# Kernel tuning notes

Hardware: AMD Instinct MI355X
Metric: run time of the kernel (lower is better)

## Reference

```python
import jax, jax.numpy as jnp
import numpy as np

EMB = 512
HEADS = 8
HEAD_DIM = EMB // HEADS


def setup_inputs() -> dict:
    key = jax.random.key(0)
    ks = jax.random.split(key, 8)
    S, B = 2048, 2
    q = jax.random.normal(ks[0], (S, B, EMB), dtype=jnp.float32)
    k = jax.random.normal(ks[1], (S, B, EMB), dtype=jnp.float32)
    v = jax.random.normal(ks[2], (S, B, EMB), dtype=jnp.float32)
    sc = 1.0 / np.sqrt(HEAD_DIM)
    Wq = jax.random.normal(ks[3], (HEAD_DIM, HEAD_DIM), dtype=jnp.float32) * sc
    Wk = jax.random.normal(ks[4], (HEAD_DIM, HEAD_DIM), dtype=jnp.float32) * sc
    Wv = jax.random.normal(ks[5], (HEAD_DIM, HEAD_DIM), dtype=jnp.float32) * sc
    Wfc = jax.random.normal(ks[6], (EMB, EMB), dtype=jnp.float32) * (1.0 / np.sqrt(EMB))
    bfc = jax.random.normal(ks[7], (EMB,), dtype=jnp.float32) * 0.01
    return {"q": q, "k": k, "v": v, "Wq": Wq, "Wk": Wk, "Wv": Wv, "Wfc": Wfc, "bfc": bfc}


def reference(q, k, v, Wq, Wk, Wv, Wfc, bfc):
    query_len, batch, emb = q.shape
    key_len = k.shape[0]
    value_len = v.shape[0]
    # Faithful to the original: plain reshape (NOT transpose) from [S,B,E] -> [B,H,S,D]
    qh = q.reshape(batch, HEADS, query_len, HEAD_DIM)
    kh = k.reshape(batch, HEADS, key_len, HEAD_DIM)
    vh = v.reshape(batch, HEADS, value_len, HEAD_DIM)
    # torch Linear(head_dim, head_dim, bias=False): y = x @ W.T
    Q = qh @ Wq.T
    K = kh @ Wk.T
    V = vh @ Wv.T
    QK = jnp.einsum('bhqd,bhkd->bhqk', Q, K)  # [B,H,S,S] score matrix (memory-bound)
    filt = jax.nn.softmax(QK / np.sqrt(HEAD_DIM).astype(np.float32), axis=3)
    att = jnp.einsum('bhqk,bhkd->bhqd', filt, V)
    att = att.reshape(query_len, batch, emb)
    return att @ Wfc.T + bfc
```

## Files before the change

### kernel.cpp

```cpp
#include <hip/hip_runtime.h>
#include <hip/hip_bf16.h>


typedef __attribute__((ext_vector_type(8))) __bf16 bf16x8;
typedef __attribute__((ext_vector_type(4))) float f32x4;
typedef __attribute__((ext_vector_type(16))) float f32x16;
typedef __attribute__((ext_vector_type(4))) unsigned short u16x4;
typedef __attribute__((ext_vector_type(4))) unsigned int u32x4;
typedef unsigned short u16;
typedef unsigned int u32;

static __device__ __forceinline__ u16 f2bf(float x) {
    u32 u = __float_as_uint(x);
    u += 0x7fff + ((u >> 16) & 1);
    return (u16)(u >> 16);
}
static __device__ __forceinline__ float bf2f(u16 h) {
    return __uint_as_float(((u32)h) << 16);
}
static __device__ __forceinline__ u32 pk2(float lo, float hi) {
    __hip_bfloat162 h2 = __float22bfloat162_rn(make_float2(lo, hi));
    u32 r; __builtin_memcpy(&r, &h2, 4); return r;
}

__global__ __launch_bounds__(256) void proj_kernel(
    const float* __restrict__ q, const float* __restrict__ k, const float* __restrict__ v,
    const float* __restrict__ Wq, const float* __restrict__ Wk, const float* __restrict__ Wv,
    const float* __restrict__ Wfc,
    u16* __restrict__ Qf, u16* __restrict__ Kf, u16* __restrict__ Vf,
    u16* __restrict__ Wb, float* __restrict__ KnSq)
{
    const int mode = blockIdx.z;
    const int t = threadIdx.x;

    if (mode == 3) {
        int i = (blockIdx.x * 256 + t) * 4;
        float4 val = *(const float4*)(Wfc + i);
        uint2 b = { pk2(val.x, val.y), pk2(val.z, val.w) };
        *(uint2*)(Wb + i) = b;
        return;
    }

    const float* A = (mode == 0) ? q : (mode == 1) ? k : v;
    const float* W = (mode == 0) ? Wq : (mode == 1) ? Wk : Wv;
    const float osc = (mode == 0) ? 0.18033688011112042f : 1.0f;

    __shared__ alignas(16) u16 Ash[128 * 88];
    __shared__ alignas(16) u16 Wsh[64 * 88];
    __shared__ float red[128];

    const int m0 = blockIdx.x * 128;
    const int w = t >> 6, l = t & 63;
    const int r16 = l & 15, q4 = l >> 4;

    {
        const float4* A4 = (const float4*)(A + (size_t)m0 * 64);
        const int c4 = t & 15;
        #pragma unroll
        for (int i = 0; i < 8; ++i) {
            int row = (t >> 4) + i * 16;
            float4 val = A4[row * 16 + c4];
            uint2 bb = { pk2(val.x, val.y), pk2(val.z, val.w) };
            *(uint2*)(Ash + row * 88 + c4 * 4) = bb;
        }
        const float4* W4 = (const float4*)W;
        #pragma unroll
        for (int i = 0; i < 4; ++i) {
            int row = (t >> 4) + i * 16;
            float4 val = W4[row * 16 + c4];
            uint2 bb = { pk2(val.x, val.y), pk2(val.z, val.w) };
            *(uint2*)(Wsh + row * 88 + c4 * 4) = bb;
        }
    }
    __syncthreads();

    bf16x8 af[2][2], wf[4][2];
    #pragma unroll
    for (int mc = 0; mc < 2; ++mc)
        #pragma unroll
        for (int kk = 0; kk < 2; ++kk)
            af[mc][kk] = *(const bf16x8*)(Ash + (w * 32 + mc * 16 + r16) * 88 + kk * 32 + q4 * 8);
    #pragma unroll
    for (int nc = 0; nc < 4; ++nc)
        #pragma unroll
        for (int kk = 0; kk < 2; ++kk)
            wf[nc][kk] = *(const bf16x8*)(Wsh + (nc * 16 + r16) * 88 + kk * 32 + q4 * 8);

    f32x4 acc[2][4];
    const f32x4 zero = {0.f, 0.f, 0.f, 0.f};
    #pragma unroll
    for (int mc = 0; mc < 2; ++mc)
        #pragma unroll
        for (int nc = 0; nc < 4; ++nc) {
            acc[mc][nc] = __builtin_amdgcn_mfma_f32_16x16x32_bf16(af[mc][0], wf[nc][0], zero, 0, 0, 0);
            acc[mc][nc] = __builtin_amdgcn_mfma_f32_16x16x32_bf16(af[mc][1], wf[nc][1], acc[mc][nc], 0, 0, 0);
        }

    __syncthreads();

    const int g = m0 >> 11, t0 = (m0 & 2047) >> 6;

    if (mode < 2) {
        #pragma unroll
        for (int mc = 0; mc < 2; ++mc)
            #pragma unroll
            for (int nc = 0; nc < 4; ++nc)
                #pragma unroll
                for (int r = 0; r < 4; ++r)
                    Ash[(w * 32 + mc * 16 + q4 * 4 + r) * 72 + nc * 16 + r16] = f2bf(acc[mc][nc][r] * osc);
        __syncthreads();
        u16* Out = (mode == 0) ? Qf : Kf;
        #pragma unroll
        for (int i = 0; i < 4; ++i) {
            int idx = i * 256 + t;
            int ll = idx & 63;
            int r = idx >> 6;
            int tl = r >> 3, c2 = (r >> 2) & 1, s = r & 3;
            int row = tl * 64 + c2 * 32 + (ll & 31);
            int col = s * 16 + (ll >> 5) * 8;
            u32x4 d = *(const u32x4*)(Ash + row * 72 + col);
            *(u32x4*)(Out + ((size_t)(((g * 32 + t0 + tl) * 2 + c2) * 4 + s) * 64 + ll) * 8) = d;
        }
        if (mode == 1) {
            if (t < 128) {
                float ss = 0.f;
                #pragma unroll
                for (int c = 0; c < 8; ++c) {
                    u32x4 d = *(const u32x4*)(Ash + t * 72 + c * 8);
                    #pragma unroll
                    for (int j = 0; j < 4; ++j) {
                        float lo = bf2f((u16)(d[j] & 0xffff));
                        float hi = bf2f((u16)(d[j] >> 16));
                        ss += lo * lo + hi * hi;
                    }
                }
                red[t] = ss;
            }
            __syncthreads();
            if (t < 64) red[t] = fmaxf(red[t], red[t + 64]);
            __syncthreads();
            if (t < 32) red[t] = fmaxf(red[t], red[t + 32]);
            __syncthreads();
            if (t == 0) {
                float mx = red[0];
                for (int i = 1; i < 32; ++i) mx = fmaxf(mx, red[i]);
                KnSq[blockIdx.x] = mx;
            }
        }
    } else {
        #pragma unroll
        for (int mc = 0; mc < 2; ++mc)
            #pragma unroll
            for (int nc = 0; nc < 4; ++nc)
                #pragma unroll
                for (int r = 0; r < 4; ++r)
                    Ash[(nc * 16 + r16) * 136 + w * 32 + mc * 16 + q4 * 4 + r] = f2bf(acc[mc][nc][r]);
        __syncthreads();
        #pragma unroll
        for (int i = 0; i < 4; ++i) {
            int idx = i * 256 + t;
            int ll = idx & 63;
            int r = idx >> 6;
            int tl = r >> 3, kh = (r >> 2) & 1, dc = (r >> 1) & 1, s2 = r & 1;
            int d = dc * 32 + (ll & 31);
            int keycol = tl * 64 + kh * 32 + s2 * 16 + (ll >> 5) * 8;
            u32x4 val = *(const u32x4*)(Ash + d * 136 + keycol);
            *(u32x4*)(Vf + ((size_t)((((g * 32 + t0 + tl) * 2 + kh) * 2 + dc) * 2 + s2) * 64 + ll) * 8) = val;
        }
    }
}

__global__ __launch_bounds__(512) void flash_kernel(
    const u16* __restrict__ Qf, const u16* __restrict__ Kf,
    const u16* __restrict__ Vf, const float* __restrict__ KnSq,
    u16* __restrict__ Att)
{
    const int bi = blockIdx.x;
    const int g = bi & 15;
    const int qt = bi >> 4;
    const int t = threadIdx.x, w = t >> 6, l = t & 63;
    const int q5 = l & 31, h = l >> 5;
    const int qs = w >> 2;
    const int kq = w & 3;
    const int kh2 = kq & 1, th = kq >> 1;

    __shared__ alignas(16) unsigned char smem[61440];
    u16* const pwRow = (u16*)smem + w * 1280 + q5 * 40;

    const u16* qbase = Qf + ((size_t)(((g * 32 + qt) * 2 + qs) * 4)) * 512 + l * 8;
    const u16* kbase = Kf + ((size_t)(((g * 32 + th * 16) * 2 + kh2) * 4)) * 512 + l * 8;
    const u16* vbase = Vf + ((size_t)((((g * 32 + th * 16) * 2 + kh2) * 2) * 2)) * 512 + l * 8;

    bf16x8 qb[4];
    #pragma unroll
    for (int s = 0; s < 4; ++s) qb[s] = *(const bf16x8*)(qbase + s * 512);

    float m;
    {
        float kss = KnSq[g * 16 + (l & 15)];
        kss = fmaxf(kss, __shfl_xor(kss, 1));
        kss = fmaxf(kss, __shfl_xor(kss, 2));
        kss = fmaxf(kss, __shfl_xor(kss, 4));
        kss = fmaxf(kss, __shfl_xor(kss, 8));
        float ss = 0.f;
        #pragma unroll
        for (int s = 0; s < 4; ++s)
            #pragma unroll
            for (int j = 0; j < 8; ++j) {
                float x = (float)qb[s][j];
                ss += x * x;
            }
        ss += __shfl_xor(ss, 32);
        m = sqrtf(ss * kss) * 1.0002f;
    }

    f32x16 mC, o0, o1, ol;
    #pragma unroll
    for (int r = 0; r < 16; ++r) { mC[r] = -m; o0[r] = 0.f; o1[r] = 0.f; ol[r] = 0.f; }

    const u16 one_bf = 0x3F80;
    bf16x8 ones;
    #pragma unroll
    for (int j = 0; j < 8; ++j) ones[j] = ((const __bf16*)&one_bf)[0];

    bf16x8 ka[4], va[4], kan[4], van[4];
    #pragma unroll
    for (int s = 0; s < 4; ++s) ka[s] = *(const bf16x8*)(kbase + s * 512);
    #pragma unroll
    for (int j = 0; j < 4; ++j) va[j] = *(const bf16x8*)(vbase + j * 512);

    for (int it = 0; it < 16; ++it) {
        const size_t nx = (size_t)((it + 1) & 15) * 4096;
        #pragma unroll
        for (int s = 0; s < 4; ++s) kan[s] = *(const bf16x8*)(kbase + nx + s * 512);
        #pragma unroll
        for (int j = 0; j < 4; ++j) van[j] = *(const bf16x8*)(vbase + nx + j * 512);

        f32x16 s;
        s = __builtin_amdgcn_mfma_f32_32x32x16_bf16(ka[0], qb[0], mC, 0, 0, 0);
        s = __builtin_amdgcn_mfma_f32_32x32x16_bf16(ka[1], qb[1], s, 0, 0, 0);
        s = __builtin_amdgcn_mfma_f32_32x32x16_bf16(ka[2], qb[2], s, 0, 0, 0);
        s = __builtin_amdgcn_mfma_f32_32x32x16_bf16(ka[3], qb[3], s, 0, 0, 0);

        float p[16];
        #pragma unroll
        for (int r = 0; r < 16; ++r) p[r] = exp2f(s[r]);

        #pragma unroll
        for (int u = 0; u < 4; ++u) {
            uint2 dd = { pk2(p[4 * u + 0], p[4 * u + 1]),
                         pk2(p[4 * u + 2], p[4 * u + 3]) };
            *(uint2*)(pwRow + u * 8 + 4 * h) = dd;
        }
        bf16x8 pb0 = *(const bf16x8*)(pwRow + (0 + h) * 8);
        bf16x8 pb1 = *(const bf16x8*)(pwRow + (2 + h) * 8);

        o0 = __builtin_amdgcn_mfma_f32_32x32x16_bf16(va[0], pb0, o0, 0, 0, 0);
        o0 = __builtin_amdgcn_mfma_f32_32x32x16_bf16(va[1], pb1, o0, 0, 0, 0);
        o1 = __builtin_amdgcn_mfma_f32_32x32x16_bf16(va[2], pb0, o1, 0, 0, 0);
        o1 = __builtin_amdgcn_mfma_f32_32x32x16_bf16(va[3], pb1, o1, 0, 0, 0);
        ol = __builtin_amdgcn_mfma_f32_32x32x16_bf16(ones, pb0, ol, 0, 0, 0);
        ol = __builtin_amdgcn_mfma_f32_32x32x16_bf16(ones, pb1, ol, 0, 0, 0);

        #pragma unroll
        for (int s2 = 0; s2 < 4; ++s2) { ka[s2] = kan[s2]; va[s2] = van[s2]; }
    }

    float psq = ol[0];

    float* const Fsh = (float*)smem;
    u16*  const Osh = (u16*)(smem + 52224);

    __syncthreads();
    if (kq != 0) {
        float* fp = Fsh + ((qs * 3) + (kq - 1)) * (64 * 34) + l * 34;
        #pragma unroll
        for (int r = 0; r < 16; ++r) { fp[r] = o0[r]; fp[16 + r] = o1[r]; }
        fp[32] = psq;
    }
    __syncthreads();
    if (kq == 0) {
        float ltot = psq;
        #pragma unroll
        for (int b = 0; b < 3; ++b) {
            const float* fp = Fsh + (qs * 3 + b) * (64 * 34) + l * 34;
            ltot += fp[32];
            #pragma unroll
            for (int r = 0; r < 16; ++r) { o0[r] += fp[r]; o1[r] += fp[16 + r]; }
        }
        float inv = 1.0f / ltot;
        const int qloc = qs * 32 + q5;
        #pragma unroll
        for (int u = 0; u < 4; ++u) {
            uint2 b0 = { pk2(o0[4*u+0] * inv, o0[4*u+1] * inv),
                         pk2(o0[4*u+2] * inv, o0[4*u+3] * inv) };
            *(uint2*)(Osh + qloc * 72 + 8 * u + 4 * h) = b0;
            uint2 b1 = { pk2(o1[4*u+0] * inv, o1[4*u+1] * inv),
                         pk2(o1[4*u+2] * inv, o1[4*u+3] * inv) };
            *(uint2*)(Osh + qloc * 72 + 32 + 8 * u + 4 * h) = b1;
        }
    }
    __syncthreads();
    {
        int row = t >> 3, cb = (t & 7) * 8;
        u16* dst = Att + ((size_t)(g * 2048 + qt * 64 + row)) * 64 + cb;
        *(u32x4*)(dst) = *(const u32x4*)(Osh + row * 72 + cb);
    }
}

__global__ __launch_bounds__(256) void fc_kernel(
    const u16* __restrict__ Att, const u16* __restrict__ Wb,
    const float* __restrict__ bfc, float* __restrict__ out)
{
    __shared__ alignas(16) u16 Ash[2][64 * 64];
    __shared__ alignas(16) u16 Wsh[2][64 * 64];

    const int t = threadIdx.x, w = t >> 6, l = t & 63;
    const int r16 = l & 15, q4 = l >> 4;
    const int r7 = r16 & 7;
    const int m0 = blockIdx.x * 64, n0 = blockIdx.y * 64;

    const int rr = t >> 3, ck = t & 7;
    const int sw0 = (ck ^ (rr & 7)) * 8;
    const int fr0 = (q4 ^ r7) * 8;
    const int fr1 = ((q4 + 4) ^ r7) * 8;

    {
        #pragma unroll
        for (int h = 0; h < 2; ++h) {
            int row = h * 32 + rr;
            *(u32x4*)(&Ash[0][row * 64 + sw0]) = *(const u32x4*)(Att + (size_t)(m0 + row) * 512 + ck * 8);
            *(u32x4*)(&Wsh[0][row * 64 + sw0]) = *(const u32x4*)(Wb + (size_t)(n0 + row) * 512 + ck * 8);
        }
    }
    __syncthreads();

    f32x4 acc[4];
    const f32x4 zero = {0.f, 0.f, 0.f, 0.f};
    #pragma unroll
    for (int nc = 0; nc < 4; ++nc) acc[nc] = zero;

    for (int it = 0; it < 8; ++it) {
        const int cur = it & 1;
        const bool hasn = (it < 7);

        u32x4 anx[2], wnx[2];
        if (hasn) {
            #pragma unroll
            for (int h = 0; h < 2; ++h) {
                int row = h * 32 + rr;
                anx[h] = *(const u32x4*)(Att + (size_t)(m0 + row) * 512 + (it + 1) * 64 + ck * 8);
                wnx[h] = *(const u32x4*)(Wb + (size_t)(n0 + row) * 512 + (it + 1) * 64 + ck * 8);
            }
        }

        bf16x8 af[2], wf[4][2];
        af[0] = *(const bf16x8*)(&Ash[cur][(w * 16 + r16) * 64 + fr0]);
        af[1] = *(const bf16x8*)(&Ash[cur][(w * 16 + r16) * 64 + fr1]);
        #pragma unroll
        for (int nc = 0; nc < 4; ++nc) {
            wf[nc][0] = *(const bf16x8*)(&Wsh[cur][(nc * 16 + r16) * 64 + fr0]);
            wf[nc][1] = *(const bf16x8*)(&Wsh[cur][(nc * 16 + r16) * 64 + fr1]);
        }

        #pragma unroll
        for (int nc = 0; nc < 4; ++nc) {
            acc[nc] = __builtin_amdgcn_mfma_f32_16x16x32_bf16(af[0], wf[nc][0], acc[nc], 0, 0, 0);
            acc[nc] = __builtin_amdgcn_mfma_f32_16x16x32_bf16(af[1], wf[nc][1], acc[nc], 0, 0, 0);
        }

        if (hasn) {
            const int nxt = cur ^ 1;
            #pragma unroll
            for (int h = 0; h < 2; ++h) {
                int row = h * 32 + rr;
                *(u32x4*)(&Ash[nxt][row * 64 + sw0]) = anx[h];
                *(u32x4*)(&Wsh[nxt][row * 64 + sw0]) = wnx[h];
            }
        }
        __syncthreads();
    }

    #pragma unroll
    for (int nc = 0; nc < 4; ++nc) {
        float bb = bfc[n0 + nc * 16 + r16];
        #pragma unroll
        for (int r = 0; r < 4; ++r) {
            int row = m0 + w * 16 + q4 * 4 + r;
            out[(size_t)row * 512 + n0 + nc * 16 + r16] = acc[nc][r] + bb;
        }
    }
}

extern "C" void kernel_launch(void* const* d_in, const int* in_sizes, int n_in,
                              void* d_out, int out_size, void* d_ws, size_t ws_size,
                              hipStream_t stream) {
    (void)in_sizes; (void)n_in; (void)out_size; (void)ws_size;
    const float* q   = (const float*)d_in[0];
    const float* k   = (const float*)d_in[1];
    const float* v   = (const float*)d_in[2];
    const float* Wq  = (const float*)d_in[3];
    const float* Wk  = (const float*)d_in[4];
    const float* Wv  = (const float*)d_in[5];
    const float* Wfc = (const float*)d_in[6];
    const float* bfc = (const float*)d_in[7];
    float* out = (float*)d_out;

    u16* Qf = (u16*)d_ws;
    u16* Kf = Qf + 2097152;
    u16* Vf = Kf + 2097152;
    u16* At = Vf + 2097152;
    u16* Wb = At + 2097152;
    float* KnSq = (float*)((char*)d_ws + 17301504);

    proj_kernel<<<dim3(256, 1, 4), 256, 0, stream>>>(q, k, v, Wq, Wk, Wv, Wfc,
                                                     Qf, Kf, Vf, Wb, KnSq);
    flash_kernel<<<dim3(512), 512, 0, stream>>>(Qf, Kf, Vf, KnSq, At);
    fc_kernel<<<dim3(64, 8), 256, 0, stream>>>(At, Wb, bfc, out);
}
```

Measured before the change: 129.2 us.

## Keep P in registers via permlane swap, drop ones-MFMA, widen fc k-step

The flash loop no longer round-trips the probability tile through LDS. It packs P to bf16 with v_cvt_pk_bf16_f32 and rearranges it across half-waves with permlane32_swap. The row-sum is now accumulated in scalar registers instead of with an extra MFMA against a ones vector. K/V prefetch double-buffering is removed and launch bounds now request 4 blocks per CU, trading load latency hiding for lower register pressure. The fc kernel processes 128-wide k chunks per barrier (halving syncs), and the key-norm reduction uses wave shuffles instead of multi-barrier LDS reduction.

```diff
diff --git a/kernel.cpp b/kernel.cpp
--- a/kernel.cpp
+++ b/kernel.cpp
@@ -7,6 +7,7 @@
 typedef __attribute__((ext_vector_type(16))) float f32x16;
 typedef __attribute__((ext_vector_type(4))) unsigned short u16x4;
 typedef __attribute__((ext_vector_type(4))) unsigned int u32x4;
+typedef __attribute__((ext_vector_type(2))) int i32x2;
 typedef unsigned short u16;
 typedef unsigned int u32;
 
@@ -21,6 +22,28 @@
 static __device__ __forceinline__ u32 pk2(float lo, float hi) {
     __hip_bfloat162 h2 = __float22bfloat162_rn(make_float2(lo, hi));
     u32 r; __builtin_memcpy(&r, &h2, 4); return r;
+}
+static __device__ __forceinline__ u32 cvtpk(float lo, float hi) {
+    u32 r;
+    asm("v_cvt_pk_bf16_f32 %0, %1, %2" : "=v"(r) : "v"(lo), "v"(hi));
+    return r;
+}
+static __device__ __forceinline__ void halfswap(u32 &x, u32 &y) {
+#if __has_builtin(__builtin_amdgcn_permlane32_swap)
+    i32x2 r = __builtin_amdgcn_permlane32_swap((int)x, (int)y, false, false);
+    x = (u32)r[0]; y = (u32)r[1];
+#else
+    int h = (threadIdx.x >> 5) & 1;
+    u32 px = (u32)__shfl_xor((int)x, 32);
+    u32 py = (u32)__shfl_xor((int)y, 32);
+    u32 nx = h ? py : x;
+    u32 ny = h ? y : px;
+    x = nx; y = ny;
+#endif
+}
+static __device__ __forceinline__ bf16x8 mk8(u32 w0, u32 w1, u32 w2, u32 w3) {
+    u32x4 u = {w0, w1, w2, w3};
+    bf16x8 r; __builtin_memcpy(&r, &u, 16); return r;
 }
 
 __global__ __launch_bounds__(256) void proj_kernel(
@@ -47,7 +70,7 @@
 
     __shared__ alignas(16) u16 Ash[128 * 88];
     __shared__ alignas(16) u16 Wsh[64 * 88];
-    __shared__ float red[128];
+    __shared__ float red[2];
 
     const int m0 = blockIdx.x * 128;
     const int w = t >> 6, l = t & 63;
@@ -122,8 +145,8 @@
             *(u32x4*)(Out + ((size_t)(((g * 32 + t0 + tl) * 2 + c2) * 4 + s) * 64 + ll) * 8) = d;
         }
         if (mode == 1) {
+            float ss = 0.f;
             if (t < 128) {
-                float ss = 0.f;
                 #pragma unroll
                 for (int c = 0; c < 8; ++c) {
                     u32x4 d = *(const u32x4*)(Ash + t * 72 + c * 8);
@@ -134,18 +157,13 @@
                         ss += lo * lo + hi * hi;
                     }
                 }
-                red[t] = ss;
             }
+            #pragma unroll
+            for (int d = 1; d < 64; d <<= 1)
+                ss = fmaxf(ss, __shfl_xor(ss, d));
+            if (t < 128 && (t & 63) == 0) red[t >> 6] = ss;
             __syncthreads();
-            if (t < 64) red[t] = fmaxf(red[t], red[t + 64]);
-            __syncthreads();
-            if (t < 32) red[t] = fmaxf(red[t], red[t + 32]);
-            __syncthreads();
-            if (t == 0) {
-                float mx = red[0];
-                for (int i = 1; i < 32; ++i) mx = fmaxf(mx, red[i]);
-                KnSq[blockIdx.x] = mx;
-            }
+            if (t == 0) KnSq[blockIdx.x] = fmaxf(red[0], red[1]);
         }
     } else {
         #pragma unroll
@@ -170,7 +188,7 @@
     }
 }
 
-__global__ __launch_bounds__(512) void flash_kernel(
+__global__ __launch_bounds__(512, 4) void flash_kernel(
     const u16* __restrict__ Qf, const u16* __restrict__ Kf,
     const u16* __restrict__ Vf, const float* __restrict__ KnSq,
     u16* __restrict__ Att)
@@ -185,7 +203,6 @@
     const int kh2 = kq & 1, th = kq >> 1;
 
     __shared__ alignas(16) unsigned char smem[61440];
-    u16* const pwRow = (u16*)smem + w * 1280 + q5 * 40;
 
     const u16* qbase = Qf + ((size_t)(((g * 32 + qt) * 2 + qs) * 4)) * 512 + l * 8;
     const u16* kbase = Kf + ((size_t)(((g * 32 + th * 16) * 2 + kh2) * 4)) * 512 + l * 8;
@@ -214,59 +231,47 @@
         m = sqrtf(ss * kss) * 1.0002f;
     }
 
-    f32x16 mC, o0, o1, ol;
-    #pragma unroll
-    for (int r = 0; r < 16; ++r) { mC[r] = -m; o0[r] = 0.f; o1[r] = 0.f; ol[r] = 0.f; }
-
-    const u16 one_bf = 0x3F80;
-    bf16x8 ones;
-    #pragma unroll
-    for (int j = 0; j < 8; ++j) ones[j] = ((const __bf16*)&one_bf)[0];
-
-    bf16x8 ka[4], va[4], kan[4], van[4];
-    #pragma unroll
-    for (int s = 0; s < 4; ++s) ka[s] = *(const bf16x8*)(kbase + s * 512);
-    #pragma unroll
-    for (int j = 0; j < 4; ++j) va[j] = *(const bf16x8*)(vbase + j * 512);
+    f32x16 mC, o0, o1;
+    #pragma unroll
+    for (int r = 0; r < 16; ++r) { mC[r] = -m; o0[r] = 0.f; o1[r] = 0.f; }
+    float ls = 0.f;
 
     for (int it = 0; it < 16; ++it) {
-        const size_t nx = (size_t)((it + 1) & 15) * 4096;
-        #pragma unroll
-        for (int s = 0; s < 4; ++s) kan[s] = *(const bf16x8*)(kbase + nx + s * 512);
-        #pragma unroll
-        for (int j = 0; j < 4; ++j) van[j] = *(const bf16x8*)(vbase + nx + j * 512);
+        const size_t ofs = (size_t)it * 4096;
+        bf16x8 ka0 = *(const bf16x8*)(kbase + ofs);
+        bf16x8 ka1 = *(const bf16x8*)(kbase + ofs + 512);
+        bf16x8 ka2 = *(const bf16x8*)(kbase + ofs + 1024);
+        bf16x8 ka3 = *(const bf16x8*)(kbase + ofs + 1536);
+        bf16x8 va0 = *(const bf16x8*)(vbase + ofs);
+        bf16x8 va1 = *(const bf16x8*)(vbase + ofs + 512);
+        bf16x8 va2 = *(const bf16x8*)(vbase + ofs + 1024);
+        bf16x8 va3 = *(const bf16x8*)(vbase + ofs + 1536);
 
         f32x16 s;
-        s = __builtin_amdgcn_mfma_f32_32x32x16_bf16(ka[0], qb[0], mC, 0, 0, 0);
-        s = __builtin_amdgcn_mfma_f32_32x32x16_bf16(ka[1], qb[1], s, 0, 0, 0);
-        s = __builtin_amdgcn_mfma_f32_32x32x16_bf16(ka[2], qb[2], s, 0, 0, 0);
-        s = __builtin_amdgcn_mfma_f32_32x32x16_bf16(ka[3], qb[3], s, 0, 0, 0);
-
-        float p[16];
-        #pragma unroll
-        for (int r = 0; r < 16; ++r) p[r] = exp2f(s[r]);
-
-        #pragma unroll
-        for (int u = 0; u < 4; ++u) {
-            uint2 dd = { pk2(p[4 * u + 0], p[4 * u + 1]),
-                         pk2(p[4 * u + 2], p[4 * u + 3]) };
-            *(uint2*)(pwRow + u * 8 + 4 * h) = dd;
-        }
-        bf16x8 pb0 = *(const bf16x8*)(pwRow + (0 + h) * 8);
-        bf16x8 pb1 = *(const bf16x8*)(pwRow + (2 + h) * 8);
-
-        o0 = __builtin_amdgcn_mfma_f32_32x32x16_bf16(va[0], pb0, o0, 0, 0, 0);
-        o0 = __builtin_amdgcn_mfma_f32_32x32x16_bf16(va[1], pb1, o0, 0, 0, 0);
-        o1 = __builtin_amdgcn_mfma_f32_32x32x16_bf16(va[2], pb0, o1, 0, 0, 0);
-        o1 = __builtin_amdgcn_mfma_f32_32x32x16_bf16(va[3], pb1, o1, 0, 0, 0);
-        ol = __builtin_amdgcn_mfma_f32_32x32x16_bf16(ones, pb0, ol, 0, 0, 0);
-        ol = __builtin_amdgcn_mfma_f32_32x32x16_bf16(ones, pb1, ol, 0, 0, 0);
-
-        #pragma unroll
-        for (int s2 = 0; s2 < 4; ++s2) { ka[s2] = kan[s2]; va[s2] = van[s2]; }
-    }
-
-    float psq = ol[0];
+        s = __builtin_amdgcn_mfma_f32_32x32x16_bf16(ka0, qb[0], mC, 0, 0, 0);
+        s = __builtin_amdgcn_mfma_f32_32x32x16_bf16(ka1, qb[1], s, 0, 0, 0);
+        s = __builtin_amdgcn_mfma_f32_32x32x16_bf16(ka2, qb[2], s, 0, 0, 0);
+        s = __builtin_amdgcn_mfma_f32_32x32x16_bf16(ka3, qb[3], s, 0, 0, 0);
+
+        #pragma unroll
+        for (int r = 0; r < 16; ++r) { s[r] = exp2f(s[r]); ls += s[r]; }
+
+        u32 a0 = cvtpk(s[0],  s[1]),  a1 = cvtpk(s[2],  s[3]);
+        u32 b0 = cvtpk(s[4],  s[5]),  b1 = cvtpk(s[6],  s[7]);
+        u32 c0 = cvtpk(s[8],  s[9]),  c1 = cvtpk(s[10], s[11]);
+        u32 d0 = cvtpk(s[12], s[13]), d1 = cvtpk(s[14], s[15]);
+        halfswap(a0, b0); halfswap(a1, b1);
+        halfswap(c0, d0); halfswap(c1, d1);
+        bf16x8 pa0 = mk8(a0, a1, b0, b1);
+        bf16x8 pa1 = mk8(c0, c1, d0, d1);
+
+        o0 = __builtin_amdgcn_mfma_f32_32x32x16_bf16(va0, pa0, o0, 0, 0, 0);
+        o0 = __builtin_amdgcn_mfma_f32_32x32x16_bf16(va1, pa1, o0, 0, 0, 0);
+        o1 = __builtin_amdgcn_mfma_f32_32x32x16_bf16(va2, pa0, o1, 0, 0, 0);
+        o1 = __builtin_amdgcn_mfma_f32_32x32x16_bf16(va3, pa1, o1, 0, 0, 0);
+    }
+
+    float psq = ls + __shfl_xor(ls, 32);
 
     float* const Fsh = (float*)smem;
     u16*  const Osh = (u16*)(smem + 52224);
@@ -292,12 +297,12 @@
         const int qloc = qs * 32 + q5;
         #pragma unroll
         for (int u = 0; u < 4; ++u) {
-            uint2 b0 = { pk2(o0[4*u+0] * inv, o0[4*u+1] * inv),
+            uint2 w0 = { pk2(o0[4*u+0] * inv, o0[4*u+1] * inv),
                          pk2(o0[4*u+2] * inv, o0[4*u+3] * inv) };
-            *(uint2*)(Osh + qloc * 72 + 8 * u + 4 * h) = b0;
-            uint2 b1 = { pk2(o1[4*u+0] * inv, o1[4*u+1] * inv),
+            *(uint2*)(Osh + qloc * 72 + 8 * u + 4 * h) = w0;
+            uint2 w1 = { pk2(o1[4*u+0] * inv, o1[4*u+1] * inv),
                          pk2(o1[4*u+2] * inv, o1[4*u+3] * inv) };
-            *(uint2*)(Osh + qloc * 72 + 32 + 8 * u + 4 * h) = b1;
+            *(uint2*)(Osh + qloc * 72 + 32 + 8 * u + 4 * h) = w1;
         }
     }
     __syncthreads();
@@ -312,8 +317,8 @@
     const u16* __restrict__ Att, const u16* __restrict__ Wb,
     const float* __restrict__ bfc, float* __restrict__ out)
 {
-    __shared__ alignas(16) u16 Ash[2][64 * 64];
-    __shared__ alignas(16) u16 Wsh[2][64 * 64];
+    __shared__ alignas(16) u16 Ash[2][2][64 * 64];
+    __shared__ alignas(16) u16 Wsh[2][2][64 * 64];
 
     const int t = threadIdx.x, w = t >> 6, l = t & 63;
     const int r16 = l & 15, q4 = l >> 4;
@@ -327,11 +332,14 @@
 
     {
         #pragma unroll
-        for (int h = 0; h < 2; ++h) {
-            int row = h * 32 + rr;
-            *(u32x4*)(&Ash[0][row * 64 + sw0]) = *(const u32x4*)(Att + (size_t)(m0 + row) * 512 + ck * 8);
-            *(u32x4*)(&Wsh[0][row * 64 + sw0]) = *(const u32x4*)(Wb + (size_t)(n0 + row) * 512 + ck * 8);
-        }
+        for (int hh = 0; hh < 2; ++hh)
+            #pragma unroll
+            for (int s = 0; s < 2; ++s) {
+                int row = hh * 32 + rr;
+                int kof = s * 64 + ck * 8;
+                *(u32x4*)(&Ash[0][s][row * 64 + sw0]) = *(const u32x4*)(Att + (size_t)(m0 + row) * 512 + kof);
+                *(u32x4*)(&Wsh[0][s][row * 64 + sw0]) = *(const u32x4*)(Wb + (size_t)(n0 + row) * 512 + kof);
+            }
     }
     __syncthreads();
 
@@ -340,43 +348,46 @@
     #pragma unroll
     for (int nc = 0; nc < 4; ++nc) acc[nc] = zero;
 
-    for (int it = 0; it < 8; ++it) {
-        const int cur = it & 1;
-        const bool hasn = (it < 7);
-
-        u32x4 anx[2], wnx[2];
+    for (int c = 0; c < 4; ++c) {
+        const int cur = c & 1;
+        const bool hasn = (c < 3);
+
+        u32x4 an[4], wn[4];
         if (hasn) {
             #pragma unroll
-            for (int h = 0; h < 2; ++h) {
-                int row = h * 32 + rr;
-                anx[h] = *(const u32x4*)(Att + (size_t)(m0 + row) * 512 + (it + 1) * 64 + ck * 8);
-                wnx[h] = *(const u32x4*)(Wb + (size_t)(n0 + row) * 512 + (it + 1) * 64 + ck * 8);
+            for (int hh = 0; hh < 2; ++hh)
+                #pragma unroll
+                for (int s = 0; s < 2; ++s) {
+                    int row = hh * 32 + rr;
+                    int kof = (c + 1) * 128 + s * 64 + ck * 8;
+                    an[hh * 2 + s] = *(const u32x4*)(Att + (size_t)(m0 + row) * 512 + kof);
+                    wn[hh * 2 + s] = *(const u32x4*)(Wb + (size_t)(n0 + row) * 512 + kof);
+                }
+        }
+
+        #pragma unroll
+        for (int s = 0; s < 2; ++s) {
+            bf16x8 af0 = *(const bf16x8*)(&Ash[cur][s][(w * 16 + r16) * 64 + fr0]);
+            bf16x8 af1 = *(const bf16x8*)(&Ash[cur][s][(w * 16 + r16) * 64 + fr1]);
+            #pragma unroll
+            for (int nc = 0; nc < 4; ++nc) {
+                bf16x8 wf0 = *(const bf16x8*)(&Wsh[cur][s][(nc * 16 + r16) * 64 + fr0]);
+                bf16x8 wf1 = *(const bf16x8*)(&Wsh[cur][s][(nc * 16 + r16) * 64 + fr1]);
+                acc[nc] = __builtin_amdgcn_mfma_f32_16x16x32_bf16(af0, wf0, acc[nc], 0, 0, 0);
+                acc[nc] = __builtin_amdgcn_mfma_f32_16x16x32_bf16(af1, wf1, acc[nc], 0, 0, 0);
             }
-        }
-
-        bf16x8 af[2], wf[4][2];
-        af[0] = *(const bf16x8*)(&Ash[cur][(w * 16 + r16) * 64 + fr0]);
-        af[1] = *(const bf16x8*)(&Ash[cur][(w * 16 + r16) * 64 + fr1]);
-        #pragma unroll
-        for (int nc = 0; nc < 4; ++nc) {
-            wf[nc][0] = *(const bf16x8*)(&Wsh[cur][(nc * 16 + r16) * 64 + fr0]);
-            wf[nc][1] = *(const bf16x8*)(&Wsh[cur][(nc * 16 + r16) * 64 + fr1]);
-        }
-
-        #pragma unroll
-        for (int nc = 0; nc < 4; ++nc) {
-            acc[nc] = __builtin_amdgcn_mfma_f32_16x16x32_bf16(af[0], wf[nc][0], acc[nc], 0, 0, 0);
-            acc[nc] = __builtin_amdgcn_mfma_f32_16x16x32_bf16(af[1], wf[nc][1], acc[nc], 0, 0, 0);
         }
 
         if (hasn) {
             const int nxt = cur ^ 1;
             #pragma unroll
-            for (int h = 0; h < 2; ++h) {
-                int row = h * 32 + rr;
-                *(u32x4*)(&Ash[nxt][row * 64 + sw0]) = anx[h];
-                *(u32x4*)(&Wsh[nxt][row * 64 + sw0]) = wnx[h];
-            }
+            for (int hh = 0; hh < 2; ++hh)
+                #pragma unroll
+                for (int s = 0; s < 2; ++s) {
+                    int row = hh * 32 + rr;
+                    *(u32x4*)(&Ash[nxt][s][row * 64 + sw0]) = an[hh * 2 + s];
+                    *(u32x4*)(&Wsh[nxt][s][row * 64 + sw0]) = wn[hh * 2 + s];
+                }
         }
         __syncthreads();
     }
```

Result: faster. 119.5 us, median of 2 (-7.5%).
